# Kernel optimization log

Measured on AMD Instinct MI355X. Metric: run time of the kernel, lower is better.

Reference implementation:

```python
import jax, jax.numpy as jnp
import numpy as np

DATA_DIM = 10000
ID_EMBED_DIM = 256
QK_DIM = 64
B, N = 4, 4096
SCALE = QK_DIM ** (-0.5)


def setup_inputs() -> dict:
    key = jax.random.key(0)
    k1, k2, k3, k4, k5, k6, k7 = jax.random.split(key, 7)
    val = jax.random.normal(k1, (B, N), dtype=jnp.float32)
    pos = jax.random.randint(k2, (B, N), 0, DATA_DIM + 1)
    # learned params (torch default inits approximated with scaled normals/uniforms)
    embed = jax.random.normal(k3, (DATA_DIM + 1, ID_EMBED_DIM), dtype=jnp.float32)
    lim = 1.0 / np.sqrt(ID_EMBED_DIM)
    Wq = jax.random.uniform(k4, (QK_DIM, ID_EMBED_DIM), minval=-lim, maxval=lim, dtype=jnp.float32)
    bq = jax.random.uniform(k5, (QK_DIM,), minval=-lim, maxval=lim, dtype=jnp.float32)
    Wk = jax.random.uniform(k6, (QK_DIM, ID_EMBED_DIM), minval=-lim, maxval=lim, dtype=jnp.float32)
    bk = jax.random.uniform(k7, (QK_DIM,), minval=-lim, maxval=lim, dtype=jnp.float32)
    return {"t": 0, "val": val, "pos": pos, "embed": embed,
            "Wq": Wq, "bq": bq, "Wk": Wk, "bk": bk}


def reference(t, val, pos, embed, Wq, bq, Wk, bk):
    # t is unused (ODE-style signature)
    id_embed = embed[pos]                              # [B, N, E] gather
    q = jnp.einsum('bne,de->bnd', id_embed, Wq) + bq   # [B, N, D]
    k = jnp.einsum('bne,de->bnd', id_embed, Wk) + bk   # [B, N, D]
    # soft_weights[b,i,j] = q[b,i,:] . k[b,j,:] * scale  (no softmax)
    soft_weights = jnp.einsum('bid,bjd->bij', q, k) * SCALE  # [B, N, N]
    fx = jnp.einsum('bij,bi->bj', soft_weights, val)         # contract over i
    return val + val * fx
```

## Files before the change

kernel.cpp:

```cpp
#include <hip/hip_runtime.h>

#define NN 4096
#define BB 4
#define EE 256
#define DD 64
#define SCALE 0.125f

#define RW1 16
#define RB1 (4 * RW1)
__global__ __launch_bounds__(256) void k_accum(
        const float* __restrict__ val, const int* __restrict__ pos,
        const float* __restrict__ embed,
        float* __restrict__ u, float* __restrict__ Vsum) {
    const int b    = blockIdx.y;
    const int t    = threadIdx.x;
    const int lane = t & 63;
    const int wv   = t >> 6;
    const int base = blockIdx.x * RB1 + wv * RW1;

    float4 acc = make_float4(0.f, 0.f, 0.f, 0.f);
    float vsum = 0.f;
    #pragma unroll 4
    for (int r = 0; r < RW1; ++r) {
        const int i = base + r;
        const float v = val[b * NN + i];
        const int   p = pos[b * NN + i];
        const float4 ev = reinterpret_cast<const float4*>(embed + (size_t)p * EE)[lane];
        acc.x += v * ev.x; acc.y += v * ev.y;
        acc.z += v * ev.z; acc.w += v * ev.w;
        vsum += v;
    }

    __shared__ float part[4][EE];
    __shared__ float vpart[4];
    *reinterpret_cast<float4*>(&part[wv][lane * 4]) = acc;
    if (lane == 0) vpart[wv] = vsum;
    __syncthreads();

    const float s = part[0][t] + part[1][t] + part[2][t] + part[3][t];
    atomicAdd(&u[b * EE + t], s);
    if (t == 0) atomicAdd(&Vsum[b], vpart[0] + vpart[1] + vpart[2] + vpart[3]);
}

#define RW2 16
#define RB2 (4 * RW2)
__global__ __launch_bounds__(256) void k_fused(
        const float* __restrict__ val, const int* __restrict__ pos,
        const float* __restrict__ embed,
        const float* __restrict__ u, const float* __restrict__ Vsum,
        const float* __restrict__ Wq, const float* __restrict__ bq,
        const float* __restrict__ Wk, const float* __restrict__ bk,
        float* __restrict__ out) {
    const int b    = blockIdx.y;
    const int t    = threadIdx.x;
    const int lane = t & 63;
    const int wv   = t >> 6;

    __shared__ float ps[4][DD];
    __shared__ float sS[DD];
    __shared__ float wsh[EE];
    __shared__ float cSh;

    {
        const int d = t & 63, seg = t >> 6;
        const float4* uu = reinterpret_cast<const float4*>(u + b * EE + seg * 64);
        const float4* wq = reinterpret_cast<const float4*>(Wq + (size_t)d * EE + seg * 64);
        float acc = 0.f;
        #pragma unroll
        for (int q = 0; q < 16; ++q) {
            const float4 a = uu[q], w4 = wq[q];
            acc += a.x * w4.x + a.y * w4.y + a.z * w4.z + a.w * w4.w;
        }
        ps[seg][d] = acc;
    }
    __syncthreads();
    if (t < DD) sS[t] = ps[0][t] + ps[1][t] + ps[2][t] + ps[3][t] + bq[t] * Vsum[b];
    __syncthreads();

    if (wv == 0) {
        float x = sS[lane] * bk[lane];
        #pragma unroll
        for (int off = 32; off > 0; off >>= 1) x += __shfl_down(x, off, 64);
        if (lane == 0) cSh = x;
    }
    {
        float acc = 0.f;
        #pragma unroll
        for (int d = 0; d < DD; ++d) acc += sS[d] * Wk[d * EE + t];
        wsh[t] = acc;
    }
    __syncthreads();

    const float4 wf = reinterpret_cast<const float4*>(wsh)[lane];
    const float  cb = cSh;
    const int j0 = blockIdx.x * RB2 + wv * RW2;
    #pragma unroll 4
    for (int r = 0; r < RW2; ++r) {
        const int j = j0 + r;
        const int p = pos[b * NN + j];
        const float4 ev = reinterpret_cast<const float4*>(embed + (size_t)p * EE)[lane];
        float acc = ev.x * wf.x + ev.y * wf.y + ev.z * wf.z + ev.w * wf.w;
        #pragma unroll
        for (int off = 32; off > 0; off >>= 1) acc += __shfl_down(acc, off, 64);
        if (lane == 0) {
            const float v = val[b * NN + j];
            out[b * NN + j] = v * (1.f + SCALE * (acc + cb));
        }
    }
}

extern "C" void kernel_launch(void* const* d_in, const int* in_sizes, int n_in,
                              void* d_out, int out_size, void* d_ws, size_t ws_size,
                              hipStream_t stream) {
    const float* val   = (const float*)d_in[1];
    const int*   pos   = (const int*)d_in[2];
    const float* embed = (const float*)d_in[3];
    const float* Wq    = (const float*)d_in[4];
    const float* bq    = (const float*)d_in[5];
    const float* Wk    = (const float*)d_in[6];
    const float* bk    = (const float*)d_in[7];
    float* out = (float*)d_out;

    float* ws = (float*)d_ws;
    float* u  = ws;
    float* V  = ws + BB * EE;

    hipMemsetAsync(u, 0, (BB * EE + BB) * sizeof(float), stream);

    dim3 g1(NN / RB1, BB);
    k_accum<<<g1, 256, 0, stream>>>(val, pos, embed, u, V);

    dim3 g2(NN / RB2, BB);
    k_fused<<<g2, 256, 0, stream>>>(val, pos, embed, u, V, Wq, bq, Wk, bk, out);
}
```

Baseline: 94.88 us.

## Replace atomic accumulation with per-block partials reduced in consumer kernel

The first kernel now writes per-block partial sums of the value-weighted embedding to workspace instead of atomically adding into a global vector. This removes the memset launch and atomic contention. Every block of the second kernel redundantly reduces the 128 partials per batch. Both kernels use smaller row tiles (32 rows per block, 8 per wave), giving more blocks. Positions and values are preloaded into registers so the gathers can issue together, and output writes are gathered through shared memory so they are coalesced. The cost is that each of the 512 second-stage blocks reads 128 KB of partials.

New measurement: 91.56 us. 1.04x faster.

```diff
diff --git a/kernel.cpp b/kernel.cpp
--- a/kernel.cpp
+++ b/kernel.cpp
@@ -5,107 +5,123 @@
 #define EE 256
 #define DD 64
 #define SCALE 0.125f
+#define NBLK 128
+#define RB 32
+#define RW 8
 
-#define RW1 16
-#define RB1 (4 * RW1)
 __global__ __launch_bounds__(256) void k_accum(
         const float* __restrict__ val, const int* __restrict__ pos,
         const float* __restrict__ embed,
-        float* __restrict__ u, float* __restrict__ Vsum) {
-    const int b    = blockIdx.y;
-    const int t    = threadIdx.x;
-    const int lane = t & 63;
-    const int wv   = t >> 6;
-    const int base = blockIdx.x * RB1 + wv * RW1;
+        float* __restrict__ part, float* __restrict__ vpart) {
+    const int b = blockIdx.y, t = threadIdx.x;
+    const int lane = t & 63, wv = t >> 6;
+    const int base = b * NN + blockIdx.x * RB + wv * RW;
+
+    float v[RW]; int p[RW];
+    #pragma unroll
+    for (int r = 0; r < RW; ++r) { v[r] = val[base + r]; p[r] = pos[base + r]; }
 
     float4 acc = make_float4(0.f, 0.f, 0.f, 0.f);
-    float vsum = 0.f;
-    #pragma unroll 4
-    for (int r = 0; r < RW1; ++r) {
-        const int i = base + r;
-        const float v = val[b * NN + i];
-        const int   p = pos[b * NN + i];
-        const float4 ev = reinterpret_cast<const float4*>(embed + (size_t)p * EE)[lane];
-        acc.x += v * ev.x; acc.y += v * ev.y;
-        acc.z += v * ev.z; acc.w += v * ev.w;
-        vsum += v;
+    float vs = 0.f;
+    #pragma unroll
+    for (int r = 0; r < RW; ++r) {
+        const float4 ev = reinterpret_cast<const float4*>(embed + (size_t)p[r] * EE)[lane];
+        acc.x += v[r] * ev.x; acc.y += v[r] * ev.y;
+        acc.z += v[r] * ev.z; acc.w += v[r] * ev.w;
+        vs += v[r];
     }
 
-    __shared__ float part[4][EE];
-    __shared__ float vpart[4];
-    *reinterpret_cast<float4*>(&part[wv][lane * 4]) = acc;
-    if (lane == 0) vpart[wv] = vsum;
+    __shared__ float plds[4][EE];
+    __shared__ float vlds[4];
+    *reinterpret_cast<float4*>(&plds[wv][4 * lane]) = acc;
+    if (lane == 0) vlds[wv] = vs;
     __syncthreads();
 
-    const float s = part[0][t] + part[1][t] + part[2][t] + part[3][t];
-    atomicAdd(&u[b * EE + t], s);
-    if (t == 0) atomicAdd(&Vsum[b], vpart[0] + vpart[1] + vpart[2] + vpart[3]);
+    const float s = plds[0][t] + plds[1][t] + plds[2][t] + plds[3][t];
+    part[((size_t)b * NBLK + blockIdx.x) * EE + t] = s;
+    if (t == 0) vpart[b * NBLK + blockIdx.x] = vlds[0] + vlds[1] + vlds[2] + vlds[3];
 }
 
-#define RW2 16
-#define RB2 (4 * RW2)
 __global__ __launch_bounds__(256) void k_fused(
         const float* __restrict__ val, const int* __restrict__ pos,
         const float* __restrict__ embed,
-        const float* __restrict__ u, const float* __restrict__ Vsum,
+        const float* __restrict__ part, const float* __restrict__ vpart,
         const float* __restrict__ Wq, const float* __restrict__ bq,
         const float* __restrict__ Wk, const float* __restrict__ bk,
         float* __restrict__ out) {
-    const int b    = blockIdx.y;
-    const int t    = threadIdx.x;
-    const int lane = t & 63;
-    const int wv   = t >> 6;
+    const int b = blockIdx.y, t = threadIdx.x;
+    const int lane = t & 63, wv = t >> 6;
 
+    __shared__ float uS[EE];
     __shared__ float ps[4][DD];
     __shared__ float sS[DD];
     __shared__ float wsh[EE];
-    __shared__ float cSh;
+    __shared__ float rowres[RB];
+    __shared__ float cSh, vS;
 
     {
-        const int d = t & 63, seg = t >> 6;
-        const float4* uu = reinterpret_cast<const float4*>(u + b * EE + seg * 64);
+        float a = 0.f;
+        const float* pp = part + (size_t)b * NBLK * EE + t;
+        #pragma unroll 8
+        for (int blk = 0; blk < NBLK; ++blk) a += pp[(size_t)blk * EE];
+        uS[t] = a;
+    }
+    if (t < 64) {
+        float x = vpart[b * NBLK + lane] + vpart[b * NBLK + 64 + lane];
+        #pragma unroll
+        for (int off = 32; off; off >>= 1) x += __shfl_down(x, off, 64);
+        if (lane == 0) vS = x;
+    }
+    __syncthreads();
+
+    {
+        const int d = lane, seg = wv;
+        const float4* uu = reinterpret_cast<const float4*>(&uS[seg * 64]);
         const float4* wq = reinterpret_cast<const float4*>(Wq + (size_t)d * EE + seg * 64);
-        float acc = 0.f;
+        float a = 0.f;
         #pragma unroll
         for (int q = 0; q < 16; ++q) {
-            const float4 a = uu[q], w4 = wq[q];
-            acc += a.x * w4.x + a.y * w4.y + a.z * w4.z + a.w * w4.w;
+            const float4 x = uu[q], y = wq[q];
+            a += x.x * y.x + x.y * y.y + x.z * y.z + x.w * y.w;
         }
-        ps[seg][d] = acc;
+        ps[seg][d] = a;
     }
     __syncthreads();
-    if (t < DD) sS[t] = ps[0][t] + ps[1][t] + ps[2][t] + ps[3][t] + bq[t] * Vsum[b];
+    if (t < DD) sS[t] = ps[0][t] + ps[1][t] + ps[2][t] + ps[3][t] + bq[t] * vS;
     __syncthreads();
 
     if (wv == 0) {
         float x = sS[lane] * bk[lane];
         #pragma unroll
-        for (int off = 32; off > 0; off >>= 1) x += __shfl_down(x, off, 64);
+        for (int off = 32; off; off >>= 1) x += __shfl_down(x, off, 64);
         if (lane == 0) cSh = x;
     }
     {
-        float acc = 0.f;
+        float a = 0.f;
         #pragma unroll
-        for (int d = 0; d < DD; ++d) acc += sS[d] * Wk[d * EE + t];
-        wsh[t] = acc;
+        for (int d = 0; d < DD; ++d) a += sS[d] * Wk[d * EE + t];
+        wsh[t] = a;
     }
     __syncthreads();
 
     const float4 wf = reinterpret_cast<const float4*>(wsh)[lane];
-    const float  cb = cSh;
-    const int j0 = blockIdx.x * RB2 + wv * RW2;
-    #pragma unroll 4
-    for (int r = 0; r < RW2; ++r) {
-        const int j = j0 + r;
-        const int p = pos[b * NN + j];
-        const float4 ev = reinterpret_cast<const float4*>(embed + (size_t)p * EE)[lane];
-        float acc = ev.x * wf.x + ev.y * wf.y + ev.z * wf.z + ev.w * wf.w;
+    const int base = b * NN + blockIdx.x * RB + wv * RW;
+    int p[RW];
+    #pragma unroll
+    for (int r = 0; r < RW; ++r) p[r] = pos[base + r];
+    #pragma unroll
+    for (int r = 0; r < RW; ++r) {
+        const float4 ev = reinterpret_cast<const float4*>(embed + (size_t)p[r] * EE)[lane];
+        float a = ev.x * wf.x + ev.y * wf.y + ev.z * wf.z + ev.w * wf.w;
         #pragma unroll
-        for (int off = 32; off > 0; off >>= 1) acc += __shfl_down(acc, off, 64);
-        if (lane == 0) {
-            const float v = val[b * NN + j];
-            out[b * NN + j] = v * (1.f + SCALE * (acc + cb));
-        }
+        for (int off = 32; off; off >>= 1) a += __shfl_down(a, off, 64);
+        if (lane == 0) rowres[wv * RW + r] = a;
+    }
+    __syncthreads();
+    if (t < RB) {
+        const int j = blockIdx.x * RB + t;
+        const float v = val[b * NN + j];
+        out[b * NN + j] = v * (1.f + SCALE * (rowres[t] + cSh));
     }
 }
 
@@ -121,15 +137,10 @@
     const float* bk    = (const float*)d_in[7];
     float* out = (float*)d_out;
 
-    float* ws = (float*)d_ws;
-    float* u  = ws;
-    float* V  = ws + BB * EE;
+    float* part  = (float*)d_ws;
+    float* vpart = part + (size_t)BB * NBLK * EE;
 
-    hipMemsetAsync(u, 0, (BB * EE + BB) * sizeof(float), stream);
-
-    dim3 g1(NN / RB1, BB);
-    k_accum<<<g1, 256, 0, stream>>>(val, pos, embed, u, V);
-
-    dim3 g2(NN / RB2, BB);
-    k_fused<<<g2, 256, 0, stream>>>(val, pos, embed, u, V, Wq, bq, Wk, bk, out);
+    dim3 g(NBLK, BB);
+    k_accum<<<g, 256, 0, stream>>>(val, pos, embed, part, vpart);
+    k_fused<<<g, 256, 0, stream>>>(val, pos, embed, part, vpart, Wq, bq, Wk, bk, out);
 }
```
